# Performance work log

Measured on AMD Instinct MI355X. Metric: run time of the kernel, lower is better.

The kernel has to match this reference:

```python
import jax, jax.numpy as jnp
import numpy as np

B, T, C, H = 128, 512, 128, 64  # batch, seq, n_embd, head_size


def setup_inputs() -> dict:
    key = jax.random.key(0)
    ks = jax.random.split(key, 6)
    s = 1.0 / np.sqrt(C)
    return {
        "x": jax.random.normal(ks[0], (B, T, C), dtype=jnp.float32),
        "Wg": jax.random.normal(ks[1], (C, C), dtype=jnp.float32) * s,
        "bg": jnp.zeros((C,), dtype=jnp.float32),
        "Wk": jax.random.normal(ks[2], (C, H), dtype=jnp.float32) * s,
        "Wq": jax.random.normal(ks[3], (C, H), dtype=jnp.float32) * s,
        "Wv": jax.random.normal(ks[4], (C, H), dtype=jnp.float32) * s,
    }


def reference(x, Wg, bg, Wk, Wq, Wv):
    # GateLayer: x * sigmoid(Linear(x))
    g = jax.nn.sigmoid(jnp.einsum('btc,cd->btd', x, Wg) + bg)
    xg = x * g
    k = jnp.einsum('btc,ch->bth', xg, Wk)
    q = jnp.einsum('btc,ch->bth', xg, Wq)
    v = jnp.einsum('btc,ch->bth', xg, Wv)
    # NOTE: original scales by C**-0.5 (n_embd), not head_size**-0.5
    scale = C ** -0.5
    wei = jnp.einsum('bqh,bkh->bqk', q, k) * scale  # [B,T,T]
    causal = jnp.tril(jnp.ones((T, T), dtype=bool))
    wei = jnp.where(causal, wei, -jnp.inf)
    wei = jax.nn.softmax(wei, axis=-1)
    # dropout is identity in eval mode
    out = jnp.einsum('bqk,bkh->bqh', wei, v)  # [B,T,H]
    return out
```

## Files before the change

### kernel.cpp

```cpp
#include <hip/hip_runtime.h>


#define BB 128
#define TB 512
#define CC 128
#define HH 64

static constexpr float SEXP2 =
    (float)(0.088388347648318447 * 1.4426950408889634);

typedef __attribute__((ext_vector_type(8))) short bf16x8;
typedef __attribute__((ext_vector_type(8))) unsigned short u16x8;
typedef __attribute__((ext_vector_type(4))) float f32x4;

__device__ inline unsigned short f2bf(float f) {
    union { float f; unsigned u; } x; x.f = f;
    unsigned r = x.u + 0x7fff + ((x.u >> 16) & 1);
    return (unsigned short)(r >> 16);
}
__device__ inline bf16x8 pack8(float4 a, float4 b) {
    bf16x8 o;
    o[0] = (short)f2bf(a.x); o[1] = (short)f2bf(a.y);
    o[2] = (short)f2bf(a.z); o[3] = (short)f2bf(a.w);
    o[4] = (short)f2bf(b.x); o[5] = (short)f2bf(b.y);
    o[6] = (short)f2bf(b.z); o[7] = (short)f2bf(b.w);
    return o;
}

__global__ void prep_weights(const float* __restrict__ Wg, const float* __restrict__ Wk,
                             const float* __restrict__ Wq, const float* __restrict__ Wv,
                             unsigned short* __restrict__ WgT, unsigned short* __restrict__ WkT,
                             unsigned short* __restrict__ WqT, unsigned short* __restrict__ WvT)
{
    int idx = blockIdx.x * 256 + threadIdx.x;
    if (idx < 16384) {
        int n = idx >> 7, k = idx & 127;
        WgT[idx] = f2bf(Wg[k * CC + n]);
    } else {
        int j = idx - 16384;
        int mtx = j >> 13;
        int r = j & 8191;
        int n = r >> 7, k = r & 127;
        const float* W = (mtx == 0) ? Wk : (mtx == 1) ? Wq : Wv;
        unsigned short* WT = (mtx == 0) ? WkT : (mtx == 1) ? WqT : WvT;
        WT[r] = f2bf(W[k * HH + n]);
    }
}

__global__ __launch_bounds__(256, 3) void gate_qkv_kernel(
    const float* __restrict__ x, const float* __restrict__ bg,
    const unsigned short* __restrict__ WgT, const unsigned short* __restrict__ WkT,
    const unsigned short* __restrict__ WqT, const unsigned short* __restrict__ WvT,
    unsigned short* __restrict__ qo, unsigned short* __restrict__ ko,
    unsigned short* __restrict__ vto)
{
    __shared__ unsigned short wlds[192 * 136];

    const int tid  = threadIdx.x;
    const int wv   = tid >> 6;
    const int lane = tid & 63;
    const int l15  = lane & 15;
    const int quad = lane >> 4;
    const int R0   = blockIdx.x * 64;
    const int row0 = R0 + 16 * wv;

#pragma unroll
    for (int it = 0; it < 8; ++it) {
        int idx = tid + 256 * it;
        int r = idx >> 4, c8 = idx & 15;
        *(u16x8*)(wlds + r * 136 + c8 * 8) = *(const u16x8*)(WgT + r * 128 + c8 * 8);
    }

    bf16x8 bx[4];
#pragma unroll
    for (int kc = 0; kc < 4; ++kc) {
        const float* p = x + (size_t)(row0 + l15) * CC + kc * 32 + quad * 8;
        float4 a = *(const float4*)p;
        float4 c = *(const float4*)(p + 4);
        bx[kc] = pack8(a, c);
    }

    __syncthreads();

    f32x4 acc[8];
#pragma unroll
    for (int nt = 0; nt < 8; ++nt) acc[nt] = (f32x4){0.f, 0.f, 0.f, 0.f};

#pragma unroll
    for (int nt = 0; nt < 8; ++nt) {
#pragma unroll
        for (int kc = 0; kc < 4; ++kc) {
            bf16x8 aw = *(const bf16x8*)(wlds + (16 * nt + l15) * 136 + kc * 32 + quad * 8);
            acc[nt] = __builtin_amdgcn_mfma_f32_16x16x32_bf16(aw, bx[kc], acc[nt], 0, 0, 0);
        }
    }

    unsigned short* sl = wlds + 128 * 136 + wv * (16 * 40);
    bf16x8 bxg[4];
#pragma unroll
    for (int kc = 0; kc < 4; ++kc) {
#pragma unroll
        for (int half = 0; half < 2; ++half) {
            int nt = 2 * kc + half;
            float4 bgv = *(const float4*)(bg + 16 * nt + 4 * quad);
            float4 xe = *(const float4*)(x + (size_t)(row0 + l15) * CC + 16 * nt + 4 * quad);
            float e0 = __expf(-(acc[nt][0] + bgv.x));
            float e1 = __expf(-(acc[nt][1] + bgv.y));
            float e2 = __expf(-(acc[nt][2] + bgv.z));
            float e3 = __expf(-(acc[nt][3] + bgv.w));
            ushort4 o;
            o.x = f2bf(xe.x * __builtin_amdgcn_rcpf(1.f + e0));
            o.y = f2bf(xe.y * __builtin_amdgcn_rcpf(1.f + e1));
            o.z = f2bf(xe.z * __builtin_amdgcn_rcpf(1.f + e2));
            o.w = f2bf(xe.w * __builtin_amdgcn_rcpf(1.f + e3));
            *(ushort4*)(sl + l15 * 40 + 16 * half + 4 * quad) = o;
        }
        bxg[kc] = *(const bf16x8*)(sl + l15 * 40 + quad * 8);
    }

    __syncthreads();

#pragma unroll
    for (int it = 0; it < 12; ++it) {
        int idx = tid + 256 * it;
        int r = idx >> 4, c8 = idx & 15;
        const unsigned short* src = (r < 64) ? (WkT + r * 128)
                                  : (r < 128) ? (WqT + (r - 64) * 128)
                                              : (WvT + (r - 128) * 128);
        *(u16x8*)(wlds + r * 136 + c8 * 8) = *(const u16x8*)(src + c8 * 8);
    }
    __syncthreads();

    const int b = R0 >> 9, t0 = R0 & 511;
    const int m = 16 * wv + l15;
#pragma unroll
    for (int pj = 0; pj < 3; ++pj) {
        f32x4 pacc[4];
#pragma unroll
        for (int nt = 0; nt < 4; ++nt) pacc[nt] = (f32x4){0.f, 0.f, 0.f, 0.f};

#pragma unroll
        for (int nt = 0; nt < 4; ++nt) {
#pragma unroll
            for (int kc = 0; kc < 4; ++kc) {
                bf16x8 aw = *(const bf16x8*)(wlds + (64 * pj + 16 * nt + l15) * 136 +
                                             kc * 32 + quad * 8);
                pacc[nt] = __builtin_amdgcn_mfma_f32_16x16x32_bf16(
                    aw, bxg[kc], pacc[nt], 0, 0, 0);
            }
        }

        if (pj < 2) {
            unsigned short* O = (pj == 0) ? ko : qo;
#pragma unroll
            for (int nt = 0; nt < 4; ++nt) {
                ushort4 h;
                h.x = f2bf(pacc[nt][0]); h.y = f2bf(pacc[nt][1]);
                h.z = f2bf(pacc[nt][2]); h.w = f2bf(pacc[nt][3]);
                *(ushort4*)(O + (size_t)(R0 + m) * HH + 16 * nt + quad * 4) = h;
            }
        } else {
#pragma unroll
            for (int nt = 0; nt < 4; ++nt) {
                unsigned short* dst =
                    vto + (size_t)b * (HH * TB) + (16 * nt + quad * 4) * TB + t0 + m;
#pragma unroll
                for (int r = 0; r < 4; ++r)
                    dst[r * TB] = f2bf(pacc[nt][r]);
            }
        }
    }
}

__global__ __launch_bounds__(256, 3) void attn_kernel(
    const unsigned short* __restrict__ q, const unsigned short* __restrict__ k,
    const unsigned short* __restrict__ vt, float* __restrict__ out)
{
    __shared__ unsigned short ks[64 * 72];
    __shared__ unsigned short vs[64 * 72];
    __shared__ unsigned short ps[64 * 76];

    const int tid  = threadIdx.x;
    const int wave = tid >> 6;
    const int lane = tid & 63;
    const int l15  = lane & 15;
    const int quad = lane >> 4;
    const int b    = blockIdx.x;
    const int qt   = 7 - blockIdx.y;
    const int q0   = qt * 64;
    const size_t base = (size_t)b * TB * HH;

    bf16x8 ones;
#pragma unroll
    for (int i = 0; i < 8; ++i) ones[i] = (short)0x3F80;

    const int r0 = tid >> 3, c8 = (tid & 7) * 8;
    const int r1 = r0 + 32;

    bf16x8 kr0 = *(const bf16x8*)(k + base + (size_t)r0 * HH + c8);
    bf16x8 kr1 = *(const bf16x8*)(k + base + (size_t)r1 * HH + c8);
    bf16x8 vr0 = *(const bf16x8*)(vt + base + (size_t)r0 * TB + c8);
    bf16x8 vr1 = *(const bf16x8*)(vt + base + (size_t)r1 * TB + c8);

    const unsigned short* qr = q + base + (size_t)(q0 + 16 * wave + l15) * HH;
    bf16x8 aq0 = *(const bf16x8*)(qr + quad * 8);
    bf16x8 aq1 = *(const bf16x8*)(qr + 32 + quad * 8);

    f32x4 o[4], lacc;
#pragma unroll
    for (int nt = 0; nt < 4; ++nt) o[nt] = (f32x4){0.f, 0.f, 0.f, 0.f};
    lacc = (f32x4){0.f, 0.f, 0.f, 0.f};

    const int nIt = qt + 1;
    for (int kt = 0; kt < nIt; ++kt) {
        __syncthreads();
        *(bf16x8*)(ks + r0 * 72 + c8) = kr0;
        *(bf16x8*)(ks + r1 * 72 + c8) = kr1;
        *(bf16x8*)(vs + r0 * 72 + c8) = vr0;
        *(bf16x8*)(vs + r1 * 72 + c8) = vr1;
        __syncthreads();

        if (kt + 1 < nIt) {
            const int k0n = (kt + 1) * 64;
            kr0 = *(const bf16x8*)(k + base + (size_t)(k0n + r0) * HH + c8);
            kr1 = *(const bf16x8*)(k + base + (size_t)(k0n + r1) * HH + c8);
            vr0 = *(const bf16x8*)(vt + base + (size_t)r0 * TB + k0n + c8);
            vr1 = *(const bf16x8*)(vt + base + (size_t)r1 * TB + k0n + c8);
        }

        bf16x8 bk0[4], bk1[4], bv0[4], bv1[4];
#pragma unroll
        for (int nt = 0; nt < 4; ++nt) {
            bk0[nt] = *(const bf16x8*)(ks + (16 * nt + l15) * 72 + quad * 8);
            bk1[nt] = *(const bf16x8*)(ks + (16 * nt + l15) * 72 + 32 + quad * 8);
            bv0[nt] = *(const bf16x8*)(vs + (16 * nt + l15) * 72 + quad * 8);
            bv1[nt] = *(const bf16x8*)(vs + (16 * nt + l15) * 72 + 32 + quad * 8);
        }

        f32x4 s[4];
#pragma unroll
        for (int nt = 0; nt < 4; ++nt) {
            f32x4 z = (f32x4){0.f, 0.f, 0.f, 0.f};
            z = __builtin_amdgcn_mfma_f32_16x16x32_bf16(bk0[nt], aq0, z, 0, 0, 0);
            z = __builtin_amdgcn_mfma_f32_16x16x32_bf16(bk1[nt], aq1, z, 0, 0, 0);
            s[nt] = z;
        }

        const bool diag = (kt == qt);
        unsigned short* pr = ps + (16 * wave + l15) * 76;
#pragma unroll
        for (int nt = 0; nt < 4; ++nt) {
            float p[4];
#pragma unroll
            for (int r = 0; r < 4; ++r) {
                float sv = s[nt][r] * SEXP2;
                if (diag && (16 * nt + 4 * quad + r) > (16 * wave + l15)) sv = -1e30f;
                p[r] = exp2f(sv);
            }
            ushort4 h;
            h.x = f2bf(p[0]); h.y = f2bf(p[1]); h.z = f2bf(p[2]); h.w = f2bf(p[3]);
            *(ushort4*)(pr + 16 * nt + 4 * quad) = h;
        }

        bf16x8 ap0 = *(const bf16x8*)(pr + quad * 8);
        bf16x8 ap1 = *(const bf16x8*)(pr + 32 + quad * 8);
        lacc = __builtin_amdgcn_mfma_f32_16x16x32_bf16(ap0, ones, lacc, 0, 0, 0);
        lacc = __builtin_amdgcn_mfma_f32_16x16x32_bf16(ap1, ones, lacc, 0, 0, 0);
#pragma unroll
        for (int nt = 0; nt < 4; ++nt) {
            o[nt] = __builtin_amdgcn_mfma_f32_16x16x32_bf16(ap0, bv0[nt], o[nt], 0, 0, 0);
            o[nt] = __builtin_amdgcn_mfma_f32_16x16x32_bf16(ap1, bv1[nt], o[nt], 0, 0, 0);
        }
    }

    float inv[4];
#pragma unroll
    for (int r = 0; r < 4; ++r) inv[r] = __builtin_amdgcn_rcpf(lacc[r]);
#pragma unroll
    for (int nt = 0; nt < 4; ++nt)
#pragma unroll
        for (int r = 0; r < 4; ++r)
            out[base + (size_t)(q0 + 16 * wave + quad * 4 + r) * HH + 16 * nt + l15] =
                o[nt][r] * inv[r];
}

extern "C" void kernel_launch(void* const* d_in, const int* in_sizes, int n_in,
                              void* d_out, int out_size, void* d_ws, size_t ws_size,
                              hipStream_t stream) {
    const float* x  = (const float*)d_in[0];
    const float* Wg = (const float*)d_in[1];
    const float* bg = (const float*)d_in[2];
    const float* Wk = (const float*)d_in[3];
    const float* Wq = (const float*)d_in[4];
    const float* Wv = (const float*)d_in[5];
    float* out = (float*)d_out;

    unsigned short* ws = (unsigned short*)d_ws;
    const size_t BTH = (size_t)BB * TB * HH;
    unsigned short* qo  = ws;
    unsigned short* ko  = ws + BTH;
    unsigned short* vto = ws + 2 * BTH;
    unsigned short* WgT = ws + 3 * BTH;
    unsigned short* WkT = WgT + 16384;
    unsigned short* WqT = WkT + 8192;
    unsigned short* WvT = WqT + 8192;

    hipLaunchKernelGGL(prep_weights, dim3(160), dim3(256), 0, stream,
                       Wg, Wk, Wq, Wv, WgT, WkT, WqT, WvT);
    hipLaunchKernelGGL(gate_qkv_kernel, dim3(BB * TB / 64), dim3(256), 0, stream,
                       x, bg, WgT, WkT, WqT, WvT, qo, ko, vto);
    hipLaunchKernelGGL(attn_kernel, dim3(BB, 8), dim3(256), 0, stream,
                       qo, ko, vto, out);
}
```

Baseline: 117.3 us.

## Fuse gate/QKV projection into attention kernel with inter-block flag synchronization

Merges the gate+QKV projection kernel and the attention kernel into one launch. Each block computes Q/K/V for its own 64-row segment and keeps Q, K and V^T in shared memory for the diagonal tile. It publishes K and V^T to global memory and sets a per-segment flag, and later blocks spin-wait on those flags before reading earlier tiles. This removes one kernel launch, the Q round trip through global memory, and the diagonal K/V reload. The cost is cross-block spin-waiting that relies on earlier blocks being scheduled, a load imbalance because the late-segment blocks do most of the work, and less prefetching of K/V inside the loop.

Measured after the change: 151.0 us. 28.7% more time.

```diff
diff --git a/kernel.cpp b/kernel.cpp
--- a/kernel.cpp
+++ b/kernel.cpp
@@ -30,9 +30,11 @@
 __global__ void prep_weights(const float* __restrict__ Wg, const float* __restrict__ Wk,
                              const float* __restrict__ Wq, const float* __restrict__ Wv,
                              unsigned short* __restrict__ WgT, unsigned short* __restrict__ WkT,
-                             unsigned short* __restrict__ WqT, unsigned short* __restrict__ WvT)
+                             unsigned short* __restrict__ WqT, unsigned short* __restrict__ WvT,
+                             int* __restrict__ flags)
 {
     int idx = blockIdx.x * 256 + threadIdx.x;
+    if (idx < 1024) flags[idx] = 0;
     if (idx < 16384) {
         int n = idx >> 7, k = idx & 127;
         WgT[idx] = f2bf(Wg[k * CC + n]);
@@ -47,22 +49,80 @@
     }
 }
 
-__global__ __launch_bounds__(256, 3) void gate_qkv_kernel(
+__device__ __forceinline__ void attn_tile(
+    const unsigned short* ks_, const unsigned short* vs_, unsigned short* ps_,
+    bf16x8 aq0, bf16x8 aq1, bf16x8 ones, bool diag,
+    f32x4* o, f32x4& lacc, int wv, int l15, int quad)
+{
+    bf16x8 bk0[4], bk1[4], bv0[4], bv1[4];
+#pragma unroll
+    for (int nt = 0; nt < 4; ++nt) {
+        bk0[nt] = *(const bf16x8*)(ks_ + (16 * nt + l15) * 72 + quad * 8);
+        bk1[nt] = *(const bf16x8*)(ks_ + (16 * nt + l15) * 72 + 32 + quad * 8);
+        bv0[nt] = *(const bf16x8*)(vs_ + (16 * nt + l15) * 72 + quad * 8);
+        bv1[nt] = *(const bf16x8*)(vs_ + (16 * nt + l15) * 72 + 32 + quad * 8);
+    }
+
+    f32x4 s[4];
+#pragma unroll
+    for (int nt = 0; nt < 4; ++nt) {
+        f32x4 z = (f32x4){0.f, 0.f, 0.f, 0.f};
+        z = __builtin_amdgcn_mfma_f32_16x16x32_bf16(bk0[nt], aq0, z, 0, 0, 0);
+        z = __builtin_amdgcn_mfma_f32_16x16x32_bf16(bk1[nt], aq1, z, 0, 0, 0);
+        s[nt] = z;
+    }
+
+    unsigned short* pr = ps_ + (16 * wv + l15) * 76;
+#pragma unroll
+    for (int nt = 0; nt < 4; ++nt) {
+        float p[4];
+#pragma unroll
+        for (int r = 0; r < 4; ++r) {
+            float sv = s[nt][r] * SEXP2;
+            if (diag && (16 * nt + 4 * quad + r) > (16 * wv + l15)) sv = -1e30f;
+            p[r] = exp2f(sv);
+        }
+        ushort4 h;
+        h.x = f2bf(p[0]); h.y = f2bf(p[1]); h.z = f2bf(p[2]); h.w = f2bf(p[3]);
+        *(ushort4*)(pr + 16 * nt + 4 * quad) = h;
+    }
+
+    bf16x8 ap0 = *(const bf16x8*)(pr + quad * 8);
+    bf16x8 ap1 = *(const bf16x8*)(pr + 32 + quad * 8);
+    lacc = __builtin_amdgcn_mfma_f32_16x16x32_bf16(ap0, ones, lacc, 0, 0, 0);
+    lacc = __builtin_amdgcn_mfma_f32_16x16x32_bf16(ap1, ones, lacc, 0, 0, 0);
+#pragma unroll
+    for (int nt = 0; nt < 4; ++nt) {
+        o[nt] = __builtin_amdgcn_mfma_f32_16x16x32_bf16(ap0, bv0[nt], o[nt], 0, 0, 0);
+        o[nt] = __builtin_amdgcn_mfma_f32_16x16x32_bf16(ap1, bv1[nt], o[nt], 0, 0, 0);
+    }
+}
+
+__global__ __launch_bounds__(256, 3) void fused_kernel(
     const float* __restrict__ x, const float* __restrict__ bg,
     const unsigned short* __restrict__ WgT, const unsigned short* __restrict__ WkT,
     const unsigned short* __restrict__ WqT, const unsigned short* __restrict__ WvT,
-    unsigned short* __restrict__ qo, unsigned short* __restrict__ ko,
-    unsigned short* __restrict__ vto)
+    unsigned short* __restrict__ ko, unsigned short* __restrict__ vto,
+    int* __restrict__ flags, float* __restrict__ out)
 {
     __shared__ unsigned short wlds[192 * 136];
+    unsigned short* ks_ = wlds;
+    unsigned short* vs_ = wlds + 4608;
+    unsigned short* qs_ = wlds + 9216;
+    unsigned short* ps_ = wlds + 13824;
 
     const int tid  = threadIdx.x;
     const int wv   = tid >> 6;
     const int lane = tid & 63;
     const int l15  = lane & 15;
     const int quad = lane >> 4;
-    const int R0   = blockIdx.x * 64;
+    const int b    = blockIdx.x;
+    const int seg  = blockIdx.y;
+    const int t0   = seg * 64;
+    const int R0   = b * 512 + t0;
     const int row0 = R0 + 16 * wv;
+    const size_t base = (size_t)b * TB * HH;
+    const int fl = b * 8 + seg;
 
 #pragma unroll
     for (int it = 0; it < 8; ++it) {
@@ -85,15 +145,13 @@
     f32x4 acc[8];
 #pragma unroll
     for (int nt = 0; nt < 8; ++nt) acc[nt] = (f32x4){0.f, 0.f, 0.f, 0.f};
-
-#pragma unroll
-    for (int nt = 0; nt < 8; ++nt) {
+#pragma unroll
+    for (int nt = 0; nt < 8; ++nt)
 #pragma unroll
         for (int kc = 0; kc < 4; ++kc) {
             bf16x8 aw = *(const bf16x8*)(wlds + (16 * nt + l15) * 136 + kc * 32 + quad * 8);
             acc[nt] = __builtin_amdgcn_mfma_f32_16x16x32_bf16(aw, bx[kc], acc[nt], 0, 0, 0);
         }
-    }
 
     unsigned short* sl = wlds + 128 * 136 + wv * (16 * 40);
     bf16x8 bxg[4];
@@ -131,78 +189,82 @@
     }
     __syncthreads();
 
-    const int b = R0 >> 9, t0 = R0 & 511;
-    const int m = 16 * wv + l15;
-#pragma unroll
-    for (int pj = 0; pj < 3; ++pj) {
-        f32x4 pacc[4];
-#pragma unroll
-        for (int nt = 0; nt < 4; ++nt) pacc[nt] = (f32x4){0.f, 0.f, 0.f, 0.f};
-
+    f32x4 pk[4], pq[4], pv[4];
+#pragma unroll
+    for (int nt = 0; nt < 4; ++nt) {
+        pk[nt] = (f32x4){0.f, 0.f, 0.f, 0.f};
+        pq[nt] = (f32x4){0.f, 0.f, 0.f, 0.f};
+        pv[nt] = (f32x4){0.f, 0.f, 0.f, 0.f};
+    }
+#pragma unroll
+    for (int nt = 0; nt < 4; ++nt)
+#pragma unroll
+        for (int kc = 0; kc < 4; ++kc) {
+            bf16x8 aw = *(const bf16x8*)(wlds + (16 * nt + l15) * 136 + kc * 32 + quad * 8);
+            pk[nt] = __builtin_amdgcn_mfma_f32_16x16x32_bf16(aw, bxg[kc], pk[nt], 0, 0, 0);
+        }
+#pragma unroll
+    for (int nt = 0; nt < 4; ++nt)
+#pragma unroll
+        for (int kc = 0; kc < 4; ++kc) {
+            bf16x8 aw = *(const bf16x8*)(wlds + (64 + 16 * nt + l15) * 136 + kc * 32 + quad * 8);
+            pq[nt] = __builtin_amdgcn_mfma_f32_16x16x32_bf16(aw, bxg[kc], pq[nt], 0, 0, 0);
+        }
+#pragma unroll
+    for (int nt = 0; nt < 4; ++nt)
+#pragma unroll
+        for (int kc = 0; kc < 4; ++kc) {
+            bf16x8 aw = *(const bf16x8*)(wlds + (128 + 16 * nt + l15) * 136 + kc * 32 + quad * 8);
+            pv[nt] = __builtin_amdgcn_mfma_f32_16x16x32_bf16(aw, bxg[kc], pv[nt], 0, 0, 0);
+        }
+
+    __syncthreads();
+
+    const int m16 = 16 * wv + l15;
+    if (seg < 7) {
 #pragma unroll
         for (int nt = 0; nt < 4; ++nt) {
-#pragma unroll
-            for (int kc = 0; kc < 4; ++kc) {
-                bf16x8 aw = *(const bf16x8*)(wlds + (64 * pj + 16 * nt + l15) * 136 +
-                                             kc * 32 + quad * 8);
-                pacc[nt] = __builtin_amdgcn_mfma_f32_16x16x32_bf16(
-                    aw, bxg[kc], pacc[nt], 0, 0, 0);
-            }
-        }
-
-        if (pj < 2) {
-            unsigned short* O = (pj == 0) ? ko : qo;
-#pragma unroll
-            for (int nt = 0; nt < 4; ++nt) {
-                ushort4 h;
-                h.x = f2bf(pacc[nt][0]); h.y = f2bf(pacc[nt][1]);
-                h.z = f2bf(pacc[nt][2]); h.w = f2bf(pacc[nt][3]);
-                *(ushort4*)(O + (size_t)(R0 + m) * HH + 16 * nt + quad * 4) = h;
-            }
-        } else {
-#pragma unroll
-            for (int nt = 0; nt < 4; ++nt) {
-                unsigned short* dst =
-                    vto + (size_t)b * (HH * TB) + (16 * nt + quad * 4) * TB + t0 + m;
-#pragma unroll
-                for (int r = 0; r < 4; ++r)
-                    dst[r * TB] = f2bf(pacc[nt][r]);
-            }
-        }
-    }
-}
-
-__global__ __launch_bounds__(256, 3) void attn_kernel(
-    const unsigned short* __restrict__ q, const unsigned short* __restrict__ k,
-    const unsigned short* __restrict__ vt, float* __restrict__ out)
-{
-    __shared__ unsigned short ks[64 * 72];
-    __shared__ unsigned short vs[64 * 72];
-    __shared__ unsigned short ps[64 * 76];
-
-    const int tid  = threadIdx.x;
-    const int wave = tid >> 6;
-    const int lane = tid & 63;
-    const int l15  = lane & 15;
-    const int quad = lane >> 4;
-    const int b    = blockIdx.x;
-    const int qt   = 7 - blockIdx.y;
-    const int q0   = qt * 64;
-    const size_t base = (size_t)b * TB * HH;
+            unsigned long long v64 =
+                (unsigned long long)f2bf(pk[nt][0]) |
+                ((unsigned long long)f2bf(pk[nt][1]) << 16) |
+                ((unsigned long long)f2bf(pk[nt][2]) << 32) |
+                ((unsigned long long)f2bf(pk[nt][3]) << 48);
+            __hip_atomic_store(
+                (unsigned long long*)(ko + (size_t)(R0 + m16) * HH + 16 * nt + 4 * quad),
+                v64, __ATOMIC_RELAXED, __HIP_MEMORY_SCOPE_AGENT);
+        }
+#pragma unroll
+        for (int nt = 0; nt < 4; ++nt)
+#pragma unroll
+            for (int r = 0; r < 4; ++r)
+                __hip_atomic_store(
+                    vto + base + (size_t)(16 * nt + 4 * quad + r) * TB + t0 + m16,
+                    f2bf(pv[nt][r]), __ATOMIC_RELAXED, __HIP_MEMORY_SCOPE_AGENT);
+    }
+#pragma unroll
+    for (int nt = 0; nt < 4; ++nt) {
+        ushort4 hk, hq;
+        hk.x = f2bf(pk[nt][0]); hk.y = f2bf(pk[nt][1]);
+        hk.z = f2bf(pk[nt][2]); hk.w = f2bf(pk[nt][3]);
+        hq.x = f2bf(pq[nt][0]); hq.y = f2bf(pq[nt][1]);
+        hq.z = f2bf(pq[nt][2]); hq.w = f2bf(pq[nt][3]);
+        *(ushort4*)(ks_ + m16 * 72 + 16 * nt + 4 * quad) = hk;
+        *(ushort4*)(qs_ + m16 * 72 + 16 * nt + 4 * quad) = hq;
+#pragma unroll
+        for (int r = 0; r < 4; ++r)
+            vs_[(16 * nt + 4 * quad + r) * 72 + m16] = f2bf(pv[nt][r]);
+    }
+
+    __syncthreads();
+
+    if (seg < 7 && tid == 0)
+        __hip_atomic_store(&flags[fl], 1, __ATOMIC_RELEASE, __HIP_MEMORY_SCOPE_AGENT);
 
     bf16x8 ones;
 #pragma unroll
     for (int i = 0; i < 8; ++i) ones[i] = (short)0x3F80;
 
-    const int r0 = tid >> 3, c8 = (tid & 7) * 8;
-    const int r1 = r0 + 32;
-
-    bf16x8 kr0 = *(const bf16x8*)(k + base + (size_t)r0 * HH + c8);
-    bf16x8 kr1 = *(const bf16x8*)(k + base + (size_t)r1 * HH + c8);
-    bf16x8 vr0 = *(const bf16x8*)(vt + base + (size_t)r0 * TB + c8);
-    bf16x8 vr1 = *(const bf16x8*)(vt + base + (size_t)r1 * TB + c8);
-
-    const unsigned short* qr = q + base + (size_t)(q0 + 16 * wave + l15) * HH;
+    const unsigned short* qr = qs_ + (16 * wv + l15) * 72;
     bf16x8 aq0 = *(const bf16x8*)(qr + quad * 8);
     bf16x8 aq1 = *(const bf16x8*)(qr + 32 + quad * 8);
 
@@ -211,66 +273,29 @@
     for (int nt = 0; nt < 4; ++nt) o[nt] = (f32x4){0.f, 0.f, 0.f, 0.f};
     lacc = (f32x4){0.f, 0.f, 0.f, 0.f};
 
-    const int nIt = qt + 1;
-    for (int kt = 0; kt < nIt; ++kt) {
+    attn_tile(ks_, vs_, ps_, aq0, aq1, ones, true, o, lacc, wv, l15, quad);
+
+    const int r0 = tid >> 3, c8v = (tid & 7) * 8;
+    const int r1 = r0 + 32;
+    for (int kt = 0; kt < seg; ++kt) {
+        if (tid == 0) {
+            while (__hip_atomic_load(&flags[b * 8 + kt], __ATOMIC_ACQUIRE,
+                                     __HIP_MEMORY_SCOPE_AGENT) == 0)
+                __builtin_amdgcn_s_sleep(2);
+        }
         __syncthreads();
-        *(bf16x8*)(ks + r0 * 72 + c8) = kr0;
-        *(bf16x8*)(ks + r1 * 72 + c8) = kr1;
-        *(bf16x8*)(vs + r0 * 72 + c8) = vr0;
-        *(bf16x8*)(vs + r1 * 72 + c8) = vr1;
+
+        bf16x8 kr0 = *(const bf16x8*)(ko + base + (size_t)(kt * 64 + r0) * HH + c8v);
+        bf16x8 kr1 = *(const bf16x8*)(ko + base + (size_t)(kt * 64 + r1) * HH + c8v);
+        bf16x8 vr0 = *(const bf16x8*)(vto + base + (size_t)r0 * TB + kt * 64 + c8v);
+        bf16x8 vr1 = *(const bf16x8*)(vto + base + (size_t)r1 * TB + kt * 64 + c8v);
+        *(bf16x8*)(ks_ + r0 * 72 + c8v) = kr0;
+        *(bf16x8*)(ks_ + r1 * 72 + c8v) = kr1;
+        *(bf16x8*)(vs_ + r0 * 72 + c8v) = vr0;
+        *(bf16x8*)(vs_ + r1 * 72 + c8v) = vr1;
         __syncthreads();
 
-        if (kt + 1 < nIt) {
-            const int k0n = (kt + 1) * 64;
-            kr0 = *(const bf16x8*)(k + base + (size_t)(k0n + r0) * HH + c8);
-            kr1 = *(const bf16x8*)(k + base + (size_t)(k0n + r1) * HH + c8);
-            vr0 = *(const bf16x8*)(vt + base + (size_t)r0 * TB + k0n + c8);
-            vr1 = *(const bf16x8*)(vt + base + (size_t)r1 * TB + k0n + c8);
-        }
-
-        bf16x8 bk0[4], bk1[4], bv0[4], bv1[4];
-#pragma unroll
-        for (int nt = 0; nt < 4; ++nt) {
-            bk0[nt] = *(const bf16x8*)(ks + (16 * nt + l15) * 72 + quad * 8);
-            bk1[nt] = *(const bf16x8*)(ks + (16 * nt + l15) * 72 + 32 + quad * 8);
-            bv0[nt] = *(const bf16x8*)(vs + (16 * nt + l15) * 72 + quad * 8);
-            bv1[nt] = *(const bf16x8*)(vs + (16 * nt + l15) * 72 + 32 + quad * 8);
-        }
-
-        f32x4 s[4];
-#pragma unroll
-        for (int nt = 0; nt < 4; ++nt) {
-            f32x4 z = (f32x4){0.f, 0.f, 0.f, 0.f};
-            z = __builtin_amdgcn_mfma_f32_16x16x32_bf16(bk0[nt], aq0, z, 0, 0, 0);
-            z = __builtin_amdgcn_mfma_f32_16x16x32_bf16(bk1[nt], aq1, z, 0, 0, 0);
-            s[nt] = z;
-        }
-
-        const bool diag = (kt == qt);
-        unsigned short* pr = ps + (16 * wave + l15) * 76;
-#pragma unroll
-        for (int nt = 0; nt < 4; ++nt) {
-            float p[4];
-#pragma unroll
-            for (int r = 0; r < 4; ++r) {
-                float sv = s[nt][r] * SEXP2;
-                if (diag && (16 * nt + 4 * quad + r) > (16 * wave + l15)) sv = -1e30f;
-                p[r] = exp2f(sv);
-            }
-            ushort4 h;
-            h.x = f2bf(p[0]); h.y = f2bf(p[1]); h.z = f2bf(p[2]); h.w = f2bf(p[3]);
-            *(ushort4*)(pr + 16 * nt + 4 * quad) = h;
-        }
-
-        bf16x8 ap0 = *(const bf16x8*)(pr + quad * 8);
-        bf16x8 ap1 = *(const bf16x8*)(pr + 32 + quad * 8);
-        lacc = __builtin_amdgcn_mfma_f32_16x16x32_bf16(ap0, ones, lacc, 0, 0, 0);
-        lacc = __builtin_amdgcn_mfma_f32_16x16x32_bf16(ap1, ones, lacc, 0, 0, 0);
-#pragma unroll
-        for (int nt = 0; nt < 4; ++nt) {
-            o[nt] = __builtin_amdgcn_mfma_f32_16x16x32_bf16(ap0, bv0[nt], o[nt], 0, 0, 0);
-            o[nt] = __builtin_amdgcn_mfma_f32_16x16x32_bf16(ap1, bv1[nt], o[nt], 0, 0, 0);
-        }
+        attn_tile(ks_, vs_, ps_, aq0, aq1, ones, false, o, lacc, wv, l15, quad);
     }
 
     float inv[4];
@@ -280,7 +305,7 @@
     for (int nt = 0; nt < 4; ++nt)
 #pragma unroll
         for (int r = 0; r < 4; ++r)
-            out[base + (size_t)(q0 + 16 * wave + quad * 4 + r) * HH + 16 * nt + l15] =
+            out[base + (size_t)(t0 + 16 * wv + quad * 4 + r) * HH + 16 * nt + l15] =
                 o[nt][r] * inv[r];
 }
 
@@ -297,18 +322,16 @@
 
     unsigned short* ws = (unsigned short*)d_ws;
     const size_t BTH = (size_t)BB * TB * HH;
-    unsigned short* qo  = ws;
-    unsigned short* ko  = ws + BTH;
-    unsigned short* vto = ws + 2 * BTH;
-    unsigned short* WgT = ws + 3 * BTH;
+    unsigned short* ko  = ws;
+    unsigned short* vto = ws + BTH;
+    unsigned short* WgT = ws + 2 * BTH;
     unsigned short* WkT = WgT + 16384;
     unsigned short* WqT = WkT + 8192;
     unsigned short* WvT = WqT + 8192;
+    int* flags = (int*)(WvT + 8192);
 
     hipLaunchKernelGGL(prep_weights, dim3(160), dim3(256), 0, stream,
-                       Wg, Wk, Wq, Wv, WgT, WkT, WqT, WvT);
-    hipLaunchKernelGGL(gate_qkv_kernel, dim3(BB * TB / 64), dim3(256), 0, stream,
-                       x, bg, WgT, WkT, WqT, WvT, qo, ko, vto);
-    hipLaunchKernelGGL(attn_kernel, dim3(BB, 8), dim3(256), 0, stream,
-                       qo, ko, vto, out);
-}
+                       Wg, Wk, Wq, Wv, WgT, WkT, WqT, WvT, flags);
+    hipLaunchKernelGGL(fused_kernel, dim3(BB, 8), dim3(256), 0, stream,
+                       x, bg, WgT, WkT, WqT, WvT, ko, vto, flags, out);
+}
```
